# Optimization experiments

Measured on AMD Instinct MI355X. Metric: run time of the kernel, lower is better.

## Reference

```python
import jax, jax.numpy as jnp
import numpy as np

N_NODES = 50000
N_EDGES = 400000
IN_DIM = 256
OUT_DIM = 64
HEADS = 2
ATTN_HIDDEN = 64
ALPHA = 0.2
TEMP = 0.55


def setup_inputs() -> dict:
    key = jax.random.key(0)
    k_x, k_src, k_dst, k_w, k_wa, k_a = jax.random.split(key, 6)
    x = jax.random.normal(k_x, (N_NODES, IN_DIM), dtype=jnp.float32)
    src = jax.random.randint(k_src, (N_EDGES,), 0, N_NODES, dtype=jnp.int32)
    dst = jnp.sort(jax.random.randint(k_dst, (N_EDGES,), 0, N_NODES, dtype=jnp.int32))
    # Glorot-uniform-like params
    def glorot(k, shape, fan_in, fan_out):
        lim = jnp.sqrt(6.0 / (fan_in + fan_out))
        return jax.random.uniform(k, shape, jnp.float32, -lim, lim)
    W = glorot(k_w, (IN_DIM, HEADS, OUT_DIM), IN_DIM, HEADS * OUT_DIM)
    W_attn = glorot(k_wa, (HEADS, 2 * OUT_DIM, ATTN_HIDDEN), 2 * OUT_DIM, ATTN_HIDDEN)
    a_vec = glorot(k_a, (HEADS, ATTN_HIDDEN), HEADS, ATTN_HIDDEN)
    return {"x": x, "W": W, "W_attn": W_attn, "a_vec": a_vec, "src": src, "dst": dst}


def reference(x, W, W_attn, a_vec, src, dst):
    N = x.shape[0]
    # node-level projection: [N, H, F]
    Wh = jnp.einsum('nd,dhf->nhf', x, W)
    # per-edge gathers
    Wh_src = Wh[src]                                   # [E, H, F]
    Wh_dst = Wh[dst]                                   # [E, H, F]
    z = jnp.concatenate([Wh_src, Wh_dst], axis=-1)     # [E, H, 2F]
    z_act = jax.nn.leaky_relu(jnp.einsum('ehf,hfc->ehc', z, W_attn), ALPHA)
    logits = jnp.einsum('ehc,hc->eh', z_act, a_vec).astype(jnp.float32) / TEMP
    # per-head segment softmax over incoming edges of each dst node
    seg_max = jax.ops.segment_max(logits, dst, num_segments=N)   # [N, H]
    ex = jnp.exp(logits - seg_max[dst])
    seg_sum = jax.ops.segment_sum(ex, dst, num_segments=N)
    alphas = (ex / (seg_sum[dst] + 1e-9)).astype(Wh_src.dtype)   # [E, H]
    # weighted scatter-sum of source messages
    out = jax.ops.segment_sum(Wh_src * alphas[..., None], dst, num_segments=N)  # [N, H, F]
    # concat=False -> mean over heads (dropout is identity at inference)
    return out.mean(axis=1)
```

## Files before the change

### kernel.cpp

```cpp
#include <hip/hip_runtime.h>
#include <hip/hip_bf16.h>
#include <math.h>

#define N_NODES 50000
#define N_EDGES 400000
#define IN_DIM 256
#define OUT_DIM 64
#define HEADS 2
#define ATTN_HIDDEN 64
#define ALPHA_SLOPE 0.2f
#define TEMP 0.55f
#define NHF 128
#define ZDIM 384

typedef __bf16 bf16x8 __attribute__((ext_vector_type(8)));
typedef float f32x4 __attribute__((ext_vector_type(4)));

__device__ __forceinline__ ushort f2bf(float f) {
    unsigned u = __float_as_uint(f);
    u = (u + 0x7fffu + ((u >> 16) & 1u)) >> 16;
    return (ushort)u;
}
__device__ __forceinline__ unsigned pack2(float a, float b) {
    return (unsigned)f2bf(a) | ((unsigned)f2bf(b) << 16);
}
__device__ __forceinline__ float bfl(unsigned u) { return __uint_as_float(u << 16); }
__device__ __forceinline__ float bfh(unsigned u) { return __uint_as_float(u & 0xffff0000u); }

__global__ __launch_bounds__(256) void k_combine(const float* __restrict__ W,
                                                 const float* __restrict__ Wa,
                                                 ushort* __restrict__ Wctf,
                                                 const int* __restrict__ dst,
                                                 int* __restrict__ seg) {
    __shared__ float col[64];
    const int b = blockIdx.x;
    const int t = threadIdx.x;
    if (b >= ZDIM) {
        int n = (b - ZDIM) * 256 + t;
        if (n > N_NODES) return;
        int lo = 0, hi = N_EDGES;
        while (lo < hi) {
            int mid = (lo + hi) >> 1;
            if (dst[mid] < n) lo = mid + 1; else hi = mid;
        }
        seg[n] = lo;
        return;
    }
    const int n = b;
    const int k = t;
    const int c = n >> 4, r16 = n & 15;
    const int kc = k >> 5, q = (k >> 3) & 3, j = k & 7;
    const size_t pos = (size_t)(((c * 8 + kc) * 64 + q * 16 + r16)) * 8 + j;

    float val;
    if (n < 128) {
        val = W[(size_t)k * NHF + n];
    } else {
        const int part = (n - 128) >> 7;
        const int idx = (n - 128) & 127;
        const int h = idx >> 6;
        const int cc = idx & 63;
        const int fb = part ? 64 : 0;
        if (t < 64) col[t] = Wa[(size_t)h * 8192 + (size_t)(fb + t) * 64 + cc];
        __syncthreads();
        const float* wr = W + (size_t)k * NHF + h * 64;
        float acc = 0.f;
#pragma unroll
        for (int f = 0; f < 64; f++) acc += wr[f] * col[f];
        val = acc;
    }
    Wctf[pos] = f2bf(val);
}

__global__ __launch_bounds__(256, 2) void k_gemm(const float* __restrict__ x,
                                                 const ushort* __restrict__ Wctf,
                                                 ushort* __restrict__ Zb) {
    const int t = threadIdx.x;
    const int w = t >> 6, lane = t & 63;
    const int q = lane >> 4, r16 = lane & 15;
    const int wid = blockIdx.x * 4 + w;
    const int row0 = wid * 32;
    if (row0 >= N_NODES) return;

    int rA0 = row0 + r16;
    int rA1 = row0 + 16 + r16;
    rA0 = rA0 < N_NODES ? rA0 : N_NODES - 1;
    rA1 = rA1 < N_NODES ? rA1 : N_NODES - 1;
    const float* xp0 = x + (size_t)rA0 * IN_DIM + q * 8;
    const float* xp1 = x + (size_t)rA1 * IN_DIM + q * 8;
    const ushort* bp = Wctf + lane * 8;

    f32x4 acc[2][24];
#pragma unroll
    for (int mt = 0; mt < 2; mt++)
#pragma unroll
        for (int c = 0; c < 24; c++) acc[mt][c] = (f32x4){0.f, 0.f, 0.f, 0.f};

#pragma unroll 1
    for (int kc = 0; kc < 8; kc++) {
        const float4 a00 = *(const float4*)(xp0 + kc * 32);
        const float4 a01 = *(const float4*)(xp0 + kc * 32 + 4);
        const float4 a10 = *(const float4*)(xp1 + kc * 32);
        const float4 a11 = *(const float4*)(xp1 + kc * 32 + 4);
        uint4 p0, p1;
        p0.x = pack2(a00.x, a00.y); p0.y = pack2(a00.z, a00.w);
        p0.z = pack2(a01.x, a01.y); p0.w = pack2(a01.z, a01.w);
        p1.x = pack2(a10.x, a10.y); p1.y = pack2(a10.z, a10.w);
        p1.z = pack2(a11.x, a11.y); p1.w = pack2(a11.z, a11.w);
        const bf16x8 af0 = *(const bf16x8*)&p0;
        const bf16x8 af1 = *(const bf16x8*)&p1;
        const ushort* bk = bp + kc * 512;
#pragma unroll
        for (int c = 0; c < 24; c++) {
            const bf16x8 bf = *(const bf16x8*)(bk + c * 4096);
            acc[0][c] = __builtin_amdgcn_mfma_f32_16x16x32_bf16(af0, bf, acc[0][c], 0, 0, 0);
            acc[1][c] = __builtin_amdgcn_mfma_f32_16x16x32_bf16(af1, bf, acc[1][c], 0, 0, 0);
        }
    }
#pragma unroll
    for (int mt = 0; mt < 2; mt++)
#pragma unroll
        for (int c = 0; c < 24; c++)
#pragma unroll
            for (int rr = 0; rr < 4; rr++) {
                const int row = row0 + mt * 16 + q * 4 + rr;
                if (row < N_NODES)
                    Zb[(size_t)row * ZDIM + c * 16 + r16] = f2bf(acc[mt][c][rr]);
            }
}

__global__ __launch_bounds__(256) void k_fused(const ushort* __restrict__ Zb,
                                               const float* __restrict__ avec,
                                               const int* __restrict__ src,
                                               const int* __restrict__ seg,
                                               float* __restrict__ out) {
    const int lane = threadIdx.x & 63;
    const int wv = threadIdx.x >> 6;
    const int g = lane >> 4, l16 = lane & 15;
    const int n = blockIdx.x * 16 + wv * 4 + g;
    if (n >= N_NODES) return;
    const int choff = 8 * l16;

    const float4 af0 = *(const float4*)(avec + choff);
    const float4 af1 = *(const float4*)(avec + choff + 4);
    const float a[8] = {af0.x, af0.y, af0.z, af0.w, af1.x, af1.y, af1.z, af1.w};

    const uint4 udv = *(const uint4*)(Zb + (size_t)n * ZDIM + 256 + choff);
    const float ud[8] = {bfl(udv.x), bfh(udv.x), bfl(udv.y), bfh(udv.y),
                         bfl(udv.z), bfh(udv.z), bfl(udv.w), bfh(udv.w)};

    const int e0 = seg[n], e1 = seg[n + 1];
    float m = -INFINITY, l = 0.f;
    float acc[8] = {0.f, 0.f, 0.f, 0.f, 0.f, 0.f, 0.f, 0.f};

    uint4 us = make_uint4(0, 0, 0, 0), wh = us;
    if (e0 < e1) {
        const int s = src[e0];
        us = *(const uint4*)(Zb + (size_t)s * ZDIM + 128 + choff);
        wh = *(const uint4*)(Zb + (size_t)s * ZDIM + choff);
    }
    for (int e = e0; e < e1; e++) {
        const uint4 cus = us, cwh = wh;
        if (e + 1 < e1) {
            const int sn = src[e + 1];
            us = *(const uint4*)(Zb + (size_t)sn * ZDIM + 128 + choff);
            wh = *(const uint4*)(Zb + (size_t)sn * ZDIM + choff);
        }
        float p;
        {
            float v0, v1, s0, s1;
            v0 = bfl(cus.x) + ud[0]; v1 = bfh(cus.x) + ud[1];
            s0 = fmaxf(v0, ALPHA_SLOPE * v0); s1 = fmaxf(v1, ALPHA_SLOPE * v1);
            p = s0 * a[0] + s1 * a[1];
            v0 = bfl(cus.y) + ud[2]; v1 = bfh(cus.y) + ud[3];
            s0 = fmaxf(v0, ALPHA_SLOPE * v0); s1 = fmaxf(v1, ALPHA_SLOPE * v1);
            p += s0 * a[2] + s1 * a[3];
            v0 = bfl(cus.z) + ud[4]; v1 = bfh(cus.z) + ud[5];
            s0 = fmaxf(v0, ALPHA_SLOPE * v0); s1 = fmaxf(v1, ALPHA_SLOPE * v1);
            p += s0 * a[4] + s1 * a[5];
            v0 = bfl(cus.w) + ud[6]; v1 = bfh(cus.w) + ud[7];
            s0 = fmaxf(v0, ALPHA_SLOPE * v0); s1 = fmaxf(v1, ALPHA_SLOPE * v1);
            p += s0 * a[6] + s1 * a[7];
        }
        p += __shfl_xor(p, 1, 64);
        p += __shfl_xor(p, 2, 64);
        p += __shfl_xor(p, 4, 64);
        const float logit = p * (1.0f / TEMP);
        const float nm = fmaxf(m, logit);
        const float sc = __expf(m - nm);
        const float wgt = __expf(logit - nm);
        l = l * sc + wgt;
        acc[0] = acc[0] * sc + wgt * bfl(cwh.x);
        acc[1] = acc[1] * sc + wgt * bfh(cwh.x);
        acc[2] = acc[2] * sc + wgt * bfl(cwh.y);
        acc[3] = acc[3] * sc + wgt * bfh(cwh.y);
        acc[4] = acc[4] * sc + wgt * bfl(cwh.z);
        acc[5] = acc[5] * sc + wgt * bfh(cwh.z);
        acc[6] = acc[6] * sc + wgt * bfl(cwh.w);
        acc[7] = acc[7] * sc + wgt * bfh(cwh.w);
        m = nm;
    }
    const float inv = 0.5f / (l + 1e-9f);
#pragma unroll
    for (int j = 0; j < 8; j++) {
        const float v = acc[j] * inv;
        acc[j] = v + __shfl_xor(v, 8, 64);
    }
    if (l16 < 8) {
        float4 o0 = make_float4(acc[0], acc[1], acc[2], acc[3]);
        float4 o1 = make_float4(acc[4], acc[5], acc[6], acc[7]);
        float* op = out + (size_t)n * 64 + choff;
        *(float4*)op = o0;
        *(float4*)(op + 4) = o1;
    }
}

extern "C" void kernel_launch(void* const* d_in, const int* in_sizes, int n_in,
                              void* d_out, int out_size, void* d_ws, size_t ws_size,
                              hipStream_t stream) {
    const float* x    = (const float*)d_in[0];
    const float* W    = (const float*)d_in[1];
    const float* Wa   = (const float*)d_in[2];
    const float* avec = (const float*)d_in[3];
    const int*   src  = (const int*)d_in[4];
    const int*   dst  = (const int*)d_in[5];
    float* out = (float*)d_out;

    ushort* Zb   = (ushort*)d_ws;
    ushort* Wctf = Zb + 19200000;
    int*    seg  = (int*)((char*)d_ws + 38596608);

    const int seg_blocks = (N_NODES + 1 + 255) / 256;
    const int gemm_waves = (N_NODES + 31) / 32;
    k_combine <<<ZDIM + seg_blocks, 256, 0, stream>>>(W, Wa, Wctf, dst, seg);
    k_gemm    <<<(gemm_waves + 3) / 4, 256, 0, stream>>>(x, Wctf, Zb);
    k_fused   <<<(N_NODES + 15) / 16, 256, 0, stream>>>(Zb, avec, src, seg, out);
}
```

Measured before the change: 173.4 us.

## Split GEMM columns across wave pairs and deepen edge-gather prefetch to two

The projection GEMM now gives each pair of waves the same 32 rows and splits the 384 output columns between them, halving the accumulator registers per wave and raising launch bounds to 3 blocks per CU. The cost is that the x rows are loaded and converted twice per block. The fused attention kernel now keeps two edges' source rows in flight instead of one, to hide gather latency on the random src accesses. This uses more registers in the fused kernel and adds some loop control.

```diff
diff --git a/kernel.cpp b/kernel.cpp
--- a/kernel.cpp
+++ b/kernel.cpp
@@ -72,29 +72,29 @@
     Wctf[pos] = f2bf(val);
 }
 
-__global__ __launch_bounds__(256, 2) void k_gemm(const float* __restrict__ x,
+__global__ __launch_bounds__(256, 3) void k_gemm(const float* __restrict__ x,
                                                  const ushort* __restrict__ Wctf,
                                                  ushort* __restrict__ Zb) {
     const int t = threadIdx.x;
     const int w = t >> 6, lane = t & 63;
     const int q = lane >> 4, r16 = lane & 15;
-    const int wid = blockIdx.x * 4 + w;
-    const int row0 = wid * 32;
-    if (row0 >= N_NODES) return;
-
-    int rA0 = row0 + r16;
-    int rA1 = row0 + 16 + r16;
+    const int chalf = (w & 1) * 12;
+    const int rowbase = blockIdx.x * 64 + (w >> 1) * 32;
+    if (rowbase >= N_NODES) return;
+
+    int rA0 = rowbase + r16;
+    int rA1 = rowbase + 16 + r16;
     rA0 = rA0 < N_NODES ? rA0 : N_NODES - 1;
     rA1 = rA1 < N_NODES ? rA1 : N_NODES - 1;
     const float* xp0 = x + (size_t)rA0 * IN_DIM + q * 8;
     const float* xp1 = x + (size_t)rA1 * IN_DIM + q * 8;
-    const ushort* bp = Wctf + lane * 8;
-
-    f32x4 acc[2][24];
+    const ushort* bp = Wctf + chalf * 4096 + lane * 8;
+
+    f32x4 acc[2][12];
 #pragma unroll
     for (int mt = 0; mt < 2; mt++)
 #pragma unroll
-        for (int c = 0; c < 24; c++) acc[mt][c] = (f32x4){0.f, 0.f, 0.f, 0.f};
+        for (int c = 0; c < 12; c++) acc[mt][c] = (f32x4){0.f, 0.f, 0.f, 0.f};
 
 #pragma unroll 1
     for (int kc = 0; kc < 8; kc++) {
@@ -111,7 +111,7 @@
         const bf16x8 af1 = *(const bf16x8*)&p1;
         const ushort* bk = bp + kc * 512;
 #pragma unroll
-        for (int c = 0; c < 24; c++) {
+        for (int c = 0; c < 12; c++) {
             const bf16x8 bf = *(const bf16x8*)(bk + c * 4096);
             acc[0][c] = __builtin_amdgcn_mfma_f32_16x16x32_bf16(af0, bf, acc[0][c], 0, 0, 0);
             acc[1][c] = __builtin_amdgcn_mfma_f32_16x16x32_bf16(af1, bf, acc[1][c], 0, 0, 0);
@@ -120,12 +120,12 @@
 #pragma unroll
     for (int mt = 0; mt < 2; mt++)
 #pragma unroll
-        for (int c = 0; c < 24; c++)
+        for (int c = 0; c < 12; c++)
 #pragma unroll
             for (int rr = 0; rr < 4; rr++) {
-                const int row = row0 + mt * 16 + q * 4 + rr;
+                const int row = rowbase + mt * 16 + q * 4 + rr;
                 if (row < N_NODES)
-                    Zb[(size_t)row * ZDIM + c * 16 + r16] = f2bf(acc[mt][c][rr]);
+                    Zb[(size_t)row * ZDIM + (chalf + c) * 16 + r16] = f2bf(acc[mt][c][rr]);
             }
 }
 
@@ -150,22 +150,11 @@
                          bfl(udv.z), bfh(udv.z), bfl(udv.w), bfh(udv.w)};
 
     const int e0 = seg[n], e1 = seg[n + 1];
+    const int cnt = e1 - e0;
     float m = -INFINITY, l = 0.f;
     float acc[8] = {0.f, 0.f, 0.f, 0.f, 0.f, 0.f, 0.f, 0.f};
 
-    uint4 us = make_uint4(0, 0, 0, 0), wh = us;
-    if (e0 < e1) {
-        const int s = src[e0];
-        us = *(const uint4*)(Zb + (size_t)s * ZDIM + 128 + choff);
-        wh = *(const uint4*)(Zb + (size_t)s * ZDIM + choff);
-    }
-    for (int e = e0; e < e1; e++) {
-        const uint4 cus = us, cwh = wh;
-        if (e + 1 < e1) {
-            const int sn = src[e + 1];
-            us = *(const uint4*)(Zb + (size_t)sn * ZDIM + 128 + choff);
-            wh = *(const uint4*)(Zb + (size_t)sn * ZDIM + choff);
-        }
+    auto step = [&](const uint4 cus, const uint4 cwh) {
         float p;
         {
             float v0, v1, s0, s1;
@@ -199,7 +188,43 @@
         acc[6] = acc[6] * sc + wgt * bfl(cwh.w);
         acc[7] = acc[7] * sc + wgt * bfh(cwh.w);
         m = nm;
-    }
+    };
+
+    uint4 us0 = make_uint4(0,0,0,0), wh0 = us0, us1 = us0, wh1 = us0;
+    if (cnt > 0) {
+        const int s = src[e0];
+        us0 = *(const uint4*)(Zb + (size_t)s * ZDIM + 128 + choff);
+        wh0 = *(const uint4*)(Zb + (size_t)s * ZDIM + choff);
+    }
+    if (cnt > 1) {
+        const int s = src[e0 + 1];
+        us1 = *(const uint4*)(Zb + (size_t)s * ZDIM + 128 + choff);
+        wh1 = *(const uint4*)(Zb + (size_t)s * ZDIM + choff);
+    }
+    int i = 0;
+    while (i < cnt) {
+        {
+            const uint4 cus = us0, cwh = wh0;
+            if (i + 2 < cnt) {
+                const int sn = src[e0 + i + 2];
+                us0 = *(const uint4*)(Zb + (size_t)sn * ZDIM + 128 + choff);
+                wh0 = *(const uint4*)(Zb + (size_t)sn * ZDIM + choff);
+            }
+            step(cus, cwh);
+        }
+        if (++i >= cnt) break;
+        {
+            const uint4 cus = us1, cwh = wh1;
+            if (i + 2 < cnt) {
+                const int sn = src[e0 + i + 2];
+                us1 = *(const uint4*)(Zb + (size_t)sn * ZDIM + 128 + choff);
+                wh1 = *(const uint4*)(Zb + (size_t)sn * ZDIM + choff);
+            }
+            step(cus, cwh);
+        }
+        ++i;
+    }
+
     const float inv = 0.5f / (l + 1e-9f);
 #pragma unroll
     for (int j = 0; j < 8; j++) {
@@ -231,8 +256,7 @@
     int*    seg  = (int*)((char*)d_ws + 38596608);
 
     const int seg_blocks = (N_NODES + 1 + 255) / 256;
-    const int gemm_waves = (N_NODES + 31) / 32;
     k_combine <<<ZDIM + seg_blocks, 256, 0, stream>>>(W, Wa, Wctf, dst, seg);
-    k_gemm    <<<(gemm_waves + 3) / 4, 256, 0, stream>>>(x, Wctf, Zb);
+    k_gemm    <<<(N_NODES + 63) / 64, 256, 0, stream>>>(x, Wctf, Zb);
     k_fused   <<<(N_NODES + 15) / 16, 256, 0, stream>>>(Zb, avec, src, seg, out);
 }
```

Result: no change. 174.9 us (+0.9%).

## Stage B tile in LDS and split GEMM columns across a 2D grid

Applied to the files above, without the earlier changes.

The GEMM now launches a 2D grid: each block covers 8 of the 24 column tiles for 128 rows. It stages that 64KB slice of the combined weight matrix into shared memory once per block instead of re-reading it from global or L2 in every wave. It also prefetches the next K-chunk of x while the MFMAs run and cuts the accumulator count from 48 to 16 vectors per thread, freeing registers. The cost is that x rows are now read three times (once per column block) and 64KB of LDS per block may limit how many blocks fit per CU.

```diff
diff --git a/kernel.cpp b/kernel.cpp
--- a/kernel.cpp
+++ b/kernel.cpp
@@ -75,33 +75,43 @@
 __global__ __launch_bounds__(256, 2) void k_gemm(const float* __restrict__ x,
                                                  const ushort* __restrict__ Wctf,
                                                  ushort* __restrict__ Zb) {
+    __shared__ __align__(16) ushort Bs[32768];
     const int t = threadIdx.x;
     const int w = t >> 6, lane = t & 63;
     const int q = lane >> 4, r16 = lane & 15;
-    const int wid = blockIdx.x * 4 + w;
-    const int row0 = wid * 32;
-    if (row0 >= N_NODES) return;
-
-    int rA0 = row0 + r16;
-    int rA1 = row0 + 16 + r16;
+    const int cbase = blockIdx.x * 8;
+    const int rowbase = blockIdx.y * 128 + w * 32;
+
+    {
+        const uint4* gs = (const uint4*)(Wctf + (size_t)blockIdx.x * 32768);
+        uint4* ls = (uint4*)Bs;
+#pragma unroll
+        for (int i = 0; i < 16; i++) ls[i * 256 + t] = gs[i * 256 + t];
+    }
+
+    int rA0 = rowbase + r16;
+    int rA1 = rowbase + 16 + r16;
     rA0 = rA0 < N_NODES ? rA0 : N_NODES - 1;
     rA1 = rA1 < N_NODES ? rA1 : N_NODES - 1;
     const float* xp0 = x + (size_t)rA0 * IN_DIM + q * 8;
     const float* xp1 = x + (size_t)rA1 * IN_DIM + q * 8;
-    const ushort* bp = Wctf + lane * 8;
-
-    f32x4 acc[2][24];
-#pragma unroll
-    for (int mt = 0; mt < 2; mt++)
-#pragma unroll
-        for (int c = 0; c < 24; c++) acc[mt][c] = (f32x4){0.f, 0.f, 0.f, 0.f};
+
+    f32x4 acc[2][8];
+#pragma unroll
+    for (int c = 0; c < 8; c++) {
+        acc[0][c] = (f32x4){0.f, 0.f, 0.f, 0.f};
+        acc[1][c] = (f32x4){0.f, 0.f, 0.f, 0.f};
+    }
+
+    float4 a00 = *(const float4*)(xp0);
+    float4 a01 = *(const float4*)(xp0 + 4);
+    float4 a10 = *(const float4*)(xp1);
+    float4 a11 = *(const float4*)(xp1 + 4);
+
+    __syncthreads();
 
 #pragma unroll 1
     for (int kc = 0; kc < 8; kc++) {
-        const float4 a00 = *(const float4*)(xp0 + kc * 32);
-        const float4 a01 = *(const float4*)(xp0 + kc * 32 + 4);
-        const float4 a10 = *(const float4*)(xp1 + kc * 32);
-        const float4 a11 = *(const float4*)(xp1 + kc * 32 + 4);
         uint4 p0, p1;
         p0.x = pack2(a00.x, a00.y); p0.y = pack2(a00.z, a00.w);
         p0.z = pack2(a01.x, a01.y); p0.w = pack2(a01.z, a01.w);
@@ -109,10 +119,16 @@
         p1.z = pack2(a11.x, a11.y); p1.w = pack2(a11.z, a11.w);
         const bf16x8 af0 = *(const bf16x8*)&p0;
         const bf16x8 af1 = *(const bf16x8*)&p1;
-        const ushort* bk = bp + kc * 512;
-#pragma unroll
-        for (int c = 0; c < 24; c++) {
-            const bf16x8 bf = *(const bf16x8*)(bk + c * 4096);
+        if (kc < 7) {
+            const int kn = (kc + 1) * 32;
+            a00 = *(const float4*)(xp0 + kn);
+            a01 = *(const float4*)(xp0 + kn + 4);
+            a10 = *(const float4*)(xp1 + kn);
+            a11 = *(const float4*)(xp1 + kn + 4);
+        }
+#pragma unroll
+        for (int c = 0; c < 8; c++) {
+            const bf16x8 bf = *(const bf16x8*)&Bs[((c * 8 + kc) * 64 + lane) * 8];
             acc[0][c] = __builtin_amdgcn_mfma_f32_16x16x32_bf16(af0, bf, acc[0][c], 0, 0, 0);
             acc[1][c] = __builtin_amdgcn_mfma_f32_16x16x32_bf16(af1, bf, acc[1][c], 0, 0, 0);
         }
@@ -120,12 +136,12 @@
 #pragma unroll
     for (int mt = 0; mt < 2; mt++)
 #pragma unroll
-        for (int c = 0; c < 24; c++)
+        for (int c = 0; c < 8; c++)
 #pragma unroll
             for (int rr = 0; rr < 4; rr++) {
-                const int row = row0 + mt * 16 + q * 4 + rr;
+                const int row = rowbase + mt * 16 + q * 4 + rr;
                 if (row < N_NODES)
-                    Zb[(size_t)row * ZDIM + c * 16 + r16] = f2bf(acc[mt][c][rr]);
+                    Zb[(size_t)row * ZDIM + (cbase + c) * 16 + r16] = f2bf(acc[mt][c][rr]);
             }
 }
 
@@ -231,8 +247,7 @@
     int*    seg  = (int*)((char*)d_ws + 38596608);
 
     const int seg_blocks = (N_NODES + 1 + 255) / 256;
-    const int gemm_waves = (N_NODES + 31) / 32;
     k_combine <<<ZDIM + seg_blocks, 256, 0, stream>>>(W, Wa, Wctf, dst, seg);
-    k_gemm    <<<(gemm_waves + 3) / 4, 256, 0, stream>>>(x, Wctf, Zb);
+    k_gemm    <<<dim3(3, (N_NODES + 127) / 128), 256, 0, stream>>>(x, Wctf, Zb);
     k_fused   <<<(N_NODES + 15) / 16, 256, 0, stream>>>(Zb, avec, src, seg, out);
 }
```

Measured after the change: 167.7 us. 3.3% less time.
